# Performance work log

Measured on AMD Instinct MI355X. Metric: run time of the kernel, lower is better.

The kernel has to match this reference:

```python
import jax, jax.numpy as jnp
import numpy as np

CHEB_K = 3  # from init_kwargs


def setup_inputs() -> dict:
    key = jax.random.key(0)
    k1, k2, k3, k4 = jax.random.split(key, 4)
    B, N, C_IN, C_OUT, D = 32, 4096, 32, 64, 16
    x = jax.random.normal(k1, (B, N, C_IN), dtype=jnp.float32)
    node_embeddings = jax.random.normal(k2, (N, D), dtype=jnp.float32)
    laplacian_mx = jnp.zeros((N, N), dtype=jnp.float32)  # unused by forward
    weights_pool = jax.random.normal(k3, (D, CHEB_K, C_IN, C_OUT), dtype=jnp.float32) * 0.1
    bias_pool = jax.random.normal(k4, (D, C_OUT), dtype=jnp.float32) * 0.1
    return {
        'x': x,
        'node_embeddings': node_embeddings,
        'laplacian_mx': laplacian_mx,
        'weights_pool': weights_pool,
        'bias_pool': bias_pool,
    }


def reference(x, node_embeddings, laplacian_mx, weights_pool, bias_pool):
    N = node_embeddings.shape[0]
    # adaptive adjacency: softmax(relu(E E^T)) over rows
    supports = jax.nn.softmax(jax.nn.relu(node_embeddings @ node_embeddings.T), axis=1)
    # Chebyshev recursion T_0=I, T_1=A, T_k = 2A T_{k-1} - T_{k-2}
    support_set = [jnp.eye(N, dtype=x.dtype), supports]
    for _ in range(2, CHEB_K):
        support_set.append(2.0 * supports @ support_set[-1] - support_set[-2])
    supports_k = jnp.stack(support_set, axis=0)  # [K, N, N]
    # per-node generated weights/bias
    weights = jnp.einsum('nd,dkio->nkio', node_embeddings, weights_pool)  # [N,K,I,O]
    bias = node_embeddings @ bias_pool  # [N, O]
    # graph propagation: [K,N,N] x [B,N,I] -> [B,K,N,I] -> [B,N,K,I]
    x_g = jnp.einsum('knm,bmc->bknc', supports_k, x).transpose(0, 2, 1, 3)
    # per-node grouped GEMM
    out = jnp.einsum('bnki,nkio->bno', x_g, weights) + bias
    return out
```

## Files before the change

### kernel.cpp

```cpp
#include <hip/hip_runtime.h>
#include <hip/hip_bf16.h>

#define N_NODES 4096
#define BATCH   32
#define CIN     32
#define COUT    64
#define DEMB    16
#define NCOL    (BATCH * CIN)
#define KIO     (3 * CIN * COUT)
#define SPLITK  3

typedef __bf16 bf16x8 __attribute__((ext_vector_type(8)));
typedef float  floatx4 __attribute__((ext_vector_type(4)));

__device__ inline void load_lds16(const void* g, void* l) {
    __builtin_amdgcn_global_load_lds(
        (const __attribute__((address_space(1))) void*)g,
        (__attribute__((address_space(3))) void*)l, 16, 0, 0);
}

__global__ __launch_bounds__(256) void compute_U_kernel(
        const float* __restrict__ E, __hip_bfloat16* __restrict__ U,
        float* __restrict__ invRow) {
    const int n0   = blockIdx.x * 8;
    const int t    = threadIdx.x;
    const int lane = t & 63, wave = t >> 6;
    __shared__ float red[4][8];

    float en[8][DEMB];
#pragma unroll
    for (int r = 0; r < 8; ++r) {
        const float4* er = (const float4*)&E[(size_t)(n0 + r) * DEMB];
        const float4 a0 = er[0], a1 = er[1], a2 = er[2], a3 = er[3];
        en[r][ 0]=a0.x; en[r][ 1]=a0.y; en[r][ 2]=a0.z; en[r][ 3]=a0.w;
        en[r][ 4]=a1.x; en[r][ 5]=a1.y; en[r][ 6]=a1.z; en[r][ 7]=a1.w;
        en[r][ 8]=a2.x; en[r][ 9]=a2.y; en[r][10]=a2.z; en[r][11]=a2.w;
        en[r][12]=a3.x; en[r][13]=a3.y; en[r][14]=a3.z; en[r][15]=a3.w;
    }

    float sum[8] = {0.f, 0.f, 0.f, 0.f, 0.f, 0.f, 0.f, 0.f};

    for (int tile = 0; tile < 16; ++tile) {
        const int c = tile * 256 + t;
        const float4* em4 = (const float4*)&E[(size_t)c * DEMB];
        const float4 b0 = em4[0], b1 = em4[1], b2 = em4[2], b3 = em4[3];
        float em[DEMB];
        em[ 0]=b0.x; em[ 1]=b0.y; em[ 2]=b0.z; em[ 3]=b0.w;
        em[ 4]=b1.x; em[ 5]=b1.y; em[ 6]=b1.z; em[ 7]=b1.w;
        em[ 8]=b2.x; em[ 9]=b2.y; em[10]=b2.z; em[11]=b2.w;
        em[12]=b3.x; em[13]=b3.y; em[14]=b3.z; em[15]=b3.w;
#pragma unroll
        for (int r = 0; r < 8; ++r) {
            float dt = 0.f;
#pragma unroll
            for (int d = 0; d < DEMB; ++d) dt += en[r][d] * em[d];
            const float ev = __expf(fmaxf(dt, 0.f));
            sum[r] += ev;
            U[(size_t)(n0 + r) * N_NODES + c] = __float2bfloat16(ev);
        }
    }
#pragma unroll
    for (int r = 0; r < 8; ++r)
#pragma unroll
        for (int off = 32; off > 0; off >>= 1) sum[r] += __shfl_xor(sum[r], off);
    if (lane == 0)
#pragma unroll
        for (int r = 0; r < 8; ++r) red[wave][r] = sum[r];
    __syncthreads();
    if (t < 8)
        invRow[n0 + t] = 1.0f / (red[0][t] + red[1][t] + red[2][t] + red[3][t]);
}

__global__ __launch_bounds__(256) void transpose_kernel(
        const float* __restrict__ x,
        __hip_bfloat16* __restrict__ Xt, __hip_bfloat16* __restrict__ Bt) {
    const int m0 = blockIdx.x * 64;
    const int b  = blockIdx.y;
    const int t  = threadIdx.x;
    __shared__ float tile[64][33];
    {
        const int ml = t >> 2, cg = (t & 3) * 8;
        const float* src = &x[((size_t)b * N_NODES + (m0 + ml)) * CIN + cg];
        const float4 r0 = *(const float4*)src;
        const float4 r1 = *(const float4*)(src + 4);
        tile[ml][cg+0] = r0.x; tile[ml][cg+1] = r0.y; tile[ml][cg+2] = r0.z; tile[ml][cg+3] = r0.w;
        tile[ml][cg+4] = r1.x; tile[ml][cg+5] = r1.y; tile[ml][cg+6] = r1.z; tile[ml][cg+7] = r1.w;
    }
    __syncthreads();
    {
        const int ml = t >> 2, cg = (t & 3) * 8;
        __hip_bfloat16* dst = &Xt[(size_t)(m0 + ml) * NCOL + b * CIN + cg];
#pragma unroll
        for (int j = 0; j < 8; ++j) dst[j] = __float2bfloat16(tile[ml][cg + j]);
    }
    {
        const int c = t >> 3, mg = (t & 7) * 8;
        __hip_bfloat16* dst = &Bt[(size_t)(b * CIN + c) * N_NODES + m0 + mg];
#pragma unroll
        for (int j = 0; j < 8; ++j) dst[j] = __float2bfloat16(tile[mg + j][c]);
    }
}

__global__ __launch_bounds__(256) void gen_w_kernel(
        const float* __restrict__ E, const float* __restrict__ Wp,
        __hip_bfloat16* __restrict__ Wn) {
    const int c   = blockIdx.x >> 3;
    const int oo0 = (blockIdx.x & 7) * 8;
    const int nc  = blockIdx.y * 64;
    const int t   = threadIdx.x;
    const int kk  = t & 31;
    const int oo  = oo0 + (t >> 5);

    __shared__ float et[64][DEMB];
    ((float4*)et)[t] = ((const float4*)&E[(size_t)nc * DEMB])[t];
    __syncthreads();

    const int srccol = (c * 32 + kk) * 64 + oo;
    float w[DEMB];
#pragma unroll
    for (int d = 0; d < DEMB; ++d) w[d] = Wp[(size_t)d * KIO + srccol];

    const int dstoff = c * 2048 + (oo >> 4) * 512 + (oo & 15) * 32 + kk;
    for (int nl = 0; nl < 64; ++nl) {
        float acc = 0.0f;
#pragma unroll
        for (int d = 0; d < DEMB; ++d) acc += et[nl][d] * w[d];
        Wn[(size_t)(nc + nl) * KIO + dstoff] = __float2bfloat16(acc);
    }
}

__global__ __launch_bounds__(256) void gemm_splitk_kernel(
        const __hip_bfloat16* __restrict__ A,
        const __hip_bfloat16* __restrict__ Bt,
        __hip_bfloat16* __restrict__ P,
        int M, int NC, int K) {
    const int t    = threadIdx.x;
    const int row0 = blockIdx.x * 128;
    const int col0 = blockIdx.y * 128;
    const int z    = blockIdx.z;
    const int iters = K >> 6;
    const int q = iters / SPLITK, rem = iters % SPLITK;
    const int it0 = z * q + (z < rem ? z : rem);
    const int it1 = it0 + q + (z < rem ? 1 : 0);

    __shared__ alignas(16) __hip_bfloat16 As[128 * 64];
    __shared__ alignas(16) __hip_bfloat16 Bs[128 * 64];
    const int lane = t & 63, wave = t >> 6;
    const int l16 = lane & 15, quad = lane >> 4;
    const int wrow = (wave >> 1) * 64, wcol = (wave & 1) * 64;
    const int xr = l16 & 7;

    floatx4 acc[4][4] = {};

    for (int it = it0; it < it1; ++it) {
        const int kb = it << 6;
        __syncthreads();
#pragma unroll
        for (int s = 0; s < 4; ++s) {
            const int gi = s * 256 + t;
            const int r  = gi >> 3;
            const int cg = (gi & 7) ^ (r & 7);
            load_lds16(&A [(size_t)(row0 + r) * K + kb + cg * 8], &As[gi * 8]);
            load_lds16(&Bt[(size_t)(col0 + r) * K + kb + cg * 8], &Bs[gi * 8]);
        }
        __syncthreads();
#pragma unroll
        for (int ks = 0; ks < 2; ++ks) {
            bf16x8 af[4], bfr[4];
#pragma unroll
            for (int i = 0; i < 4; ++i)
                af[i]  = *(const bf16x8*)&As[(wrow + i * 16 + l16) * 64 +
                                             (((ks * 4 + quad) ^ xr) * 8)];
#pragma unroll
            for (int i = 0; i < 4; ++i)
                bfr[i] = *(const bf16x8*)&Bs[(wcol + i * 16 + l16) * 64 +
                                             (((ks * 4 + quad) ^ xr) * 8)];
#pragma unroll
            for (int i = 0; i < 4; ++i)
#pragma unroll
                for (int j = 0; j < 4; ++j)
                    acc[i][j] = __builtin_amdgcn_mfma_f32_16x16x32_bf16(
                                    af[i], bfr[j], acc[i][j], 0, 0, 0);
        }
    }

    __hip_bfloat16* Pz = P + (size_t)z * M * NC;
#pragma unroll
    for (int i = 0; i < 4; ++i)
#pragma unroll
        for (int j = 0; j < 4; ++j)
#pragma unroll
            for (int r = 0; r < 4; ++r) {
                const int rg = row0 + wrow + i * 16 + quad * 4 + r;
                const int cg = col0 + wcol + j * 16 + l16;
                Pz[(size_t)rg * NC + cg] = __float2bfloat16(acc[i][j][r]);
            }
}

__global__ __launch_bounds__(256) void combine1_kernel(
        const __hip_bfloat16* __restrict__ P, const float* __restrict__ invRow,
        __hip_bfloat16* __restrict__ Y, __hip_bfloat16* __restrict__ Yt,
        int M, int NC) {
    const int c0 = blockIdx.x * 64, m0 = blockIdx.y * 64;
    const int t = threadIdx.x;
    __shared__ float tile[64][65];
    const size_t stride = (size_t)M * NC;
#pragma unroll
    for (int j = 0; j < 16; ++j) {
        const int lin = t + j * 256;
        const int r = lin >> 6, c = lin & 63;
        const size_t idx = (size_t)(m0 + r) * NC + c0 + c;
        float s = 0.f;
#pragma unroll
        for (int z = 0; z < SPLITK; ++z) s += __bfloat162float(P[idx + z * stride]);
        s *= invRow[m0 + r];
        tile[r][c] = s;
        Y[idx] = __float2bfloat16(s);
    }
    __syncthreads();
#pragma unroll
    for (int j = 0; j < 16; ++j) {
        const int lin = t + j * 256;
        const int c = lin >> 6, r = lin & 63;
        Yt[(size_t)(c0 + c) * M + m0 + r] = __float2bfloat16(tile[r][c]);
    }
}

__global__ __launch_bounds__(256) void combine2_kernel(
        const __hip_bfloat16* __restrict__ P, const float* __restrict__ invRow,
        const __hip_bfloat16* __restrict__ sub, __hip_bfloat16* __restrict__ Y2,
        int M, int NC) {
    const size_t stride = (size_t)M * NC;
    const size_t idx0 = (size_t)blockIdx.x * 4096 + threadIdx.x;
#pragma unroll
    for (int j = 0; j < 16; ++j) {
        const size_t idx = idx0 + (size_t)j * 256;
        float s = 0.f;
#pragma unroll
        for (int z = 0; z < SPLITK; ++z) s += __bfloat162float(P[idx + z * stride]);
        s *= invRow[idx >> 10];
        Y2[idx] = __float2bfloat16(2.0f * s - __bfloat162float(sub[idx]));
    }
}

__global__ __launch_bounds__(256) void final_kernel(
        const __hip_bfloat16* __restrict__ Xt, const __hip_bfloat16* __restrict__ Y1,
        const __hip_bfloat16* __restrict__ Y2, const __hip_bfloat16* __restrict__ Wn,
        const float* __restrict__ E, const float* __restrict__ bias_pool,
        float* __restrict__ out) {
    const int t    = threadIdx.x;
    const int lane = t & 63, wave = t >> 6;
    const int l16  = lane & 15, quad = lane >> 4;
    const int n    = blockIdx.x * 4 + wave;

    const __hip_bfloat16* srcs[3] = {Xt, Y1, Y2};
    const __hip_bfloat16* Wnode = Wn + (size_t)n * KIO;

    floatx4 acc[2][4] = {};

#pragma unroll
    for (int c = 0; c < 3; ++c) {
        bf16x8 af[2];
#pragma unroll
        for (int mt = 0; mt < 2; ++mt)
            af[mt] = *(const bf16x8*)&srcs[c][(size_t)n * NCOL +
                                              (mt * 16 + l16) * 32 + quad * 8];
#pragma unroll
        for (int ot = 0; ot < 4; ++ot) {
            const bf16x8 bfr = *(const bf16x8*)&Wnode[(size_t)c * 2048 +
                                                      ot * 512 + l16 * 32 + quad * 8];
#pragma unroll
            for (int mt = 0; mt < 2; ++mt)
                acc[mt][ot] = __builtin_amdgcn_mfma_f32_16x16x32_bf16(
                                  af[mt], bfr, acc[mt][ot], 0, 0, 0);
        }
    }

    float en[DEMB];
#pragma unroll
    for (int d = 0; d < DEMB; ++d) en[d] = E[(size_t)n * DEMB + d];
#pragma unroll
    for (int ot = 0; ot < 4; ++ot) {
        float bv = 0.f;
        const int o = ot * 16 + l16;
#pragma unroll
        for (int d = 0; d < DEMB; ++d) bv += en[d] * bias_pool[d * COUT + o];
#pragma unroll
        for (int mt = 0; mt < 2; ++mt)
#pragma unroll
            for (int r = 0; r < 4; ++r) {
                const int b = mt * 16 + quad * 4 + r;
                out[((size_t)b * N_NODES + n) * COUT + o] = acc[mt][ot][r] + bv;
            }
    }
}

extern "C" void kernel_launch(void* const* d_in, const int* in_sizes, int n_in,
                              void* d_out, int out_size, void* d_ws, size_t ws_size,
                              hipStream_t stream) {
    (void)in_sizes; (void)n_in; (void)out_size; (void)ws_size;
    const float* x  = (const float*)d_in[0];
    const float* E  = (const float*)d_in[1];
    const float* Wp = (const float*)d_in[3];
    const float* bp = (const float*)d_in[4];
    float* out = (float*)d_out;

    char* ws = (char*)d_ws;
    __hip_bfloat16* U   = (__hip_bfloat16*)(ws);
    __hip_bfloat16* Xt  = (__hip_bfloat16*)(ws + 33554432);
    __hip_bfloat16* Bt1 = (__hip_bfloat16*)(ws + 41943040);
    __hip_bfloat16* Y1  = (__hip_bfloat16*)(ws + 50331648);
    __hip_bfloat16* Y1t = (__hip_bfloat16*)(ws + 58720256);
    __hip_bfloat16* P   = (__hip_bfloat16*)(ws + 67108864);
    float*       invRow = (float*)(ws + 67108864 + 25165824);
    __hip_bfloat16* Wn  = (__hip_bfloat16*)(ws + 67108864);

    compute_U_kernel<<<N_NODES / 8, 256, 0, stream>>>(E, U, invRow);
    transpose_kernel<<<dim3(N_NODES / 64, BATCH), 256, 0, stream>>>(x, Xt, Bt1);
    gemm_splitk_kernel<<<dim3(N_NODES / 128, NCOL / 128, SPLITK), 256, 0, stream>>>(
        U, Bt1, P, N_NODES, NCOL, N_NODES);
    combine1_kernel<<<dim3(NCOL / 64, N_NODES / 64), 256, 0, stream>>>(
        P, invRow, Y1, Y1t, N_NODES, NCOL);
    gemm_splitk_kernel<<<dim3(N_NODES / 128, NCOL / 128, SPLITK), 256, 0, stream>>>(
        U, Y1t, P, N_NODES, NCOL, N_NODES);
    combine2_kernel<<<dim3(N_NODES * NCOL / 4096), 256, 0, stream>>>(
        P, invRow, Xt, Bt1, N_NODES, NCOL);
    gen_w_kernel<<<dim3(24, N_NODES / 64), 256, 0, stream>>>(E, Wp, Wn);
    final_kernel<<<N_NODES / 4, 256, 0, stream>>>(Xt, Y1, Bt1, Wn, E, bp, out);
}
```

Baseline: 289.9 us.

## Triple-buffer split-K GEMM with larger 256x128 tiles and async LDS prefetch

Rewrites the propagation GEMM so each block computes a 256x128 tile with 512 threads. Global-to-LDS loads for tiles two steps ahead go into a three-buffer ring, and waits use explicit vmcnt counters with MFMA phases raised in priority, so loads overlap compute instead of being serialized by barriers. Split-K drops from 3 to 2, which cuts partial-sum traffic but leaves only 256 blocks. The large LDS footprint limits occupancy to one block per CU.

```diff
diff --git a/kernel.cpp b/kernel.cpp
--- a/kernel.cpp
+++ b/kernel.cpp
@@ -8,7 +8,7 @@
 #define DEMB    16
 #define NCOL    (BATCH * CIN)
 #define KIO     (3 * CIN * COUT)
-#define SPLITK  3
+#define SPLITK  2
 
 typedef __bf16 bf16x8 __attribute__((ext_vector_type(8)));
 typedef float  floatx4 __attribute__((ext_vector_type(4)));
@@ -129,59 +129,111 @@
     }
 }
 
-__global__ __launch_bounds__(256) void gemm_splitk_kernel(
+#define GBM 256
+#define GBN 128
+#define GBK 64
+#define NBUF 3
+
+__global__ __launch_bounds__(512, 2) void gemm_splitk_kernel(
         const __hip_bfloat16* __restrict__ A,
         const __hip_bfloat16* __restrict__ Bt,
         __hip_bfloat16* __restrict__ P,
         int M, int NC, int K) {
     const int t    = threadIdx.x;
-    const int row0 = blockIdx.x * 128;
-    const int col0 = blockIdx.y * 128;
+    const int row0 = blockIdx.x * GBM;
+    const int col0 = blockIdx.y * GBN;
     const int z    = blockIdx.z;
-    const int iters = K >> 6;
-    const int q = iters / SPLITK, rem = iters % SPLITK;
-    const int it0 = z * q + (z < rem ? z : rem);
-    const int it1 = it0 + q + (z < rem ? 1 : 0);
-
-    __shared__ alignas(16) __hip_bfloat16 As[128 * 64];
-    __shared__ alignas(16) __hip_bfloat16 Bs[128 * 64];
+    const int NT   = (K >> 6) / SPLITK;
+    const int kb0  = z * NT * GBK;
+
+    __shared__ alignas(16) __hip_bfloat16 As[NBUF][GBM * GBK];
+    __shared__ alignas(16) __hip_bfloat16 Bs[NBUF][GBN * GBK];
+
     const int lane = t & 63, wave = t >> 6;
     const int l16 = lane & 15, quad = lane >> 4;
-    const int wrow = (wave >> 1) * 64, wcol = (wave & 1) * 64;
+    const int wr = wave >> 1, wc = wave & 1;
+    const int wrow = wr * 64, wcol = wc * 64;
     const int xr = l16 & 7;
 
+    auto stageA = [&](int buf, int kb, int s) {
+        const int gi = s * 512 + t;
+        const int r  = gi >> 3;
+        const int cg = (gi & 7) ^ (r & 7);
+        load_lds16(&A[(size_t)(row0 + r) * K + kb + cg * 8], &As[buf][gi * 8]);
+    };
+    auto stageB = [&](int buf, int kb, int s) {
+        const int gi = s * 512 + t;
+        const int r  = gi >> 3;
+        const int cg = (gi & 7) ^ (r & 7);
+        load_lds16(&Bt[(size_t)(col0 + r) * K + kb + cg * 8], &Bs[buf][gi * 8]);
+    };
+
     floatx4 acc[4][4] = {};
 
-    for (int it = it0; it < it1; ++it) {
-        const int kb = it << 6;
-        __syncthreads();
-#pragma unroll
-        for (int s = 0; s < 4; ++s) {
-            const int gi = s * 256 + t;
-            const int r  = gi >> 3;
-            const int cg = (gi & 7) ^ (r & 7);
-            load_lds16(&A [(size_t)(row0 + r) * K + kb + cg * 8], &As[gi * 8]);
-            load_lds16(&Bt[(size_t)(col0 + r) * K + kb + cg * 8], &Bs[gi * 8]);
-        }
-        __syncthreads();
-#pragma unroll
-        for (int ks = 0; ks < 2; ++ks) {
-            bf16x8 af[4], bfr[4];
-#pragma unroll
-            for (int i = 0; i < 4; ++i)
-                af[i]  = *(const bf16x8*)&As[(wrow + i * 16 + l16) * 64 +
-                                             (((ks * 4 + quad) ^ xr) * 8)];
-#pragma unroll
-            for (int i = 0; i < 4; ++i)
-                bfr[i] = *(const bf16x8*)&Bs[(wcol + i * 16 + l16) * 64 +
-                                             (((ks * 4 + quad) ^ xr) * 8)];
-#pragma unroll
-            for (int i = 0; i < 4; ++i)
-#pragma unroll
-                for (int j = 0; j < 4; ++j)
-                    acc[i][j] = __builtin_amdgcn_mfma_f32_16x16x32_bf16(
-                                    af[i], bfr[j], acc[i][j], 0, 0, 0);
-        }
+#pragma unroll
+    for (int s = 0; s < 4; ++s) stageA(0, kb0, s);
+#pragma unroll
+    for (int s = 0; s < 2; ++s) stageB(0, kb0, s);
+#pragma unroll
+    for (int s = 0; s < 4; ++s) stageA(1, kb0 + GBK, s);
+#pragma unroll
+    for (int s = 0; s < 2; ++s) stageB(1, kb0 + GBK, s);
+    asm volatile("s_waitcnt vmcnt(6)" ::: "memory");
+    __builtin_amdgcn_s_barrier();
+    __builtin_amdgcn_sched_barrier(0);
+
+    int cur = 0;
+    for (int tt = 0; tt < NT; ++tt) {
+        const int  nb  = (cur + 2 >= NBUF) ? cur + 2 - NBUF : cur + 2;
+        const int  kbn = kb0 + (tt + 2) * GBK;
+        const bool pf  = (tt + 2 < NT);
+
+        bf16x8 af0[4], bf0[4];
+#pragma unroll
+        for (int i = 0; i < 4; ++i)
+            af0[i] = *(const bf16x8*)&As[cur][(wrow + i * 16 + l16) * GBK +
+                                             ((quad ^ xr) * 8)];
+#pragma unroll
+        for (int j = 0; j < 4; ++j)
+            bf0[j] = *(const bf16x8*)&Bs[cur][(wcol + j * 16 + l16) * GBK +
+                                             ((quad ^ xr) * 8)];
+        if (pf) { stageA(nb, kbn, 0); stageA(nb, kbn, 1); stageB(nb, kbn, 0); }
+        __builtin_amdgcn_s_barrier();
+        __builtin_amdgcn_s_setprio(1);
+#pragma unroll
+        for (int i = 0; i < 4; ++i)
+#pragma unroll
+            for (int j = 0; j < 4; ++j)
+                acc[i][j] = __builtin_amdgcn_mfma_f32_16x16x32_bf16(
+                                af0[i], bf0[j], acc[i][j], 0, 0, 0);
+        __builtin_amdgcn_s_setprio(0);
+        __builtin_amdgcn_s_barrier();
+
+        bf16x8 af1[4], bf1[4];
+#pragma unroll
+        for (int i = 0; i < 4; ++i)
+            af1[i] = *(const bf16x8*)&As[cur][(wrow + i * 16 + l16) * GBK +
+                                             (((4 + quad) ^ xr) * 8)];
+#pragma unroll
+        for (int j = 0; j < 4; ++j)
+            bf1[j] = *(const bf16x8*)&Bs[cur][(wcol + j * 16 + l16) * GBK +
+                                             (((4 + quad) ^ xr) * 8)];
+        if (pf) { stageA(nb, kbn, 2); stageA(nb, kbn, 3); stageB(nb, kbn, 1); }
+        __builtin_amdgcn_s_barrier();
+        __builtin_amdgcn_s_setprio(1);
+#pragma unroll
+        for (int i = 0; i < 4; ++i)
+#pragma unroll
+            for (int j = 0; j < 4; ++j)
+                acc[i][j] = __builtin_amdgcn_mfma_f32_16x16x32_bf16(
+                                af1[i], bf1[j], acc[i][j], 0, 0, 0);
+        __builtin_amdgcn_s_setprio(0);
+        if (pf) asm volatile("s_waitcnt vmcnt(6)" ::: "memory");
+        else    asm volatile("s_waitcnt vmcnt(0)" ::: "memory");
+        __builtin_amdgcn_s_barrier();
+        __builtin_amdgcn_sched_barrier(0);
+
+        cur = (cur + 1 == NBUF) ? 0 : cur + 1;
     }
 
     __hip_bfloat16* Pz = P + (size_t)z * M * NC;
@@ -317,11 +369,11 @@
 
     compute_U_kernel<<<N_NODES / 8, 256, 0, stream>>>(E, U, invRow);
     transpose_kernel<<<dim3(N_NODES / 64, BATCH), 256, 0, stream>>>(x, Xt, Bt1);
-    gemm_splitk_kernel<<<dim3(N_NODES / 128, NCOL / 128, SPLITK), 256, 0, stream>>>(
+    gemm_splitk_kernel<<<dim3(N_NODES / GBM, NCOL / GBN, SPLITK), 512, 0, stream>>>(
         U, Bt1, P, N_NODES, NCOL, N_NODES);
     combine1_kernel<<<dim3(NCOL / 64, N_NODES / 64), 256, 0, stream>>>(
         P, invRow, Y1, Y1t, N_NODES, NCOL);
-    gemm_splitk_kernel<<<dim3(N_NODES / 128, NCOL / 128, SPLITK), 256, 0, stream>>>(
+    gemm_splitk_kernel<<<dim3(N_NODES / GBM, NCOL / GBN, SPLITK), 512, 0, stream>>>(
         U, Y1t, P, N_NODES, NCOL, N_NODES);
     combine2_kernel<<<dim3(N_NODES * NCOL / 4096), 256, 0, stream>>>(
         P, invRow, Xt, Bt1, N_NODES, NCOL);
```

After: 270.2 us. 6.8% less time.
